# Performance work log

Hardware: AMD Instinct MI355X
Metric: run time of the kernel (lower is better)

Reference implementation:

```python
import jax, jax.numpy as jnp
import numpy as np

BN_EPS = 1e-5


def setup_inputs() -> dict:
    key = jax.random.key(0)
    ks = jax.random.split(key, 13)
    B, C, H, W = 32, 256, 96, 48
    return {
        "x": jax.random.normal(ks[0], (B, C, H, W), dtype=jnp.float32),
        "g_w": jax.random.normal(ks[1], (C,), dtype=jnp.float32),
        "g_b": jax.random.normal(ks[2], (1,), dtype=jnp.float32),
        "theta_w": jax.random.normal(ks[3], (C,), dtype=jnp.float32),
        "theta_b": jax.random.normal(ks[4], (1,), dtype=jnp.float32),
        "phi_w": jax.random.normal(ks[5], (C,), dtype=jnp.float32),
        "phi_b": jax.random.normal(ks[6], (1,), dtype=jnp.float32),
        "W_w": jax.random.normal(ks[7], (C,), dtype=jnp.float32),
        "W_b": jax.random.normal(ks[8], (C,), dtype=jnp.float32),
        "bn_gamma": jax.random.normal(ks[9], (C,), dtype=jnp.float32),
        "bn_beta": jax.random.normal(ks[10], (C,), dtype=jnp.float32),
        "bn_mean": jax.random.normal(ks[11], (C,), dtype=jnp.float32),
        "bn_var": jax.random.uniform(ks[12], (C,), dtype=jnp.float32),
    }


def reference(x, g_w, g_b, theta_w, theta_b, phi_w, phi_b, W_w, W_b,
              bn_gamma, bn_beta, bn_mean, bn_var):
    # x: (B, C, H, W); inter_channels == 1 so all 1x1 convs are channel dots.
    B, C, H, Wd = x.shape
    N = H * Wd
    xf = x.reshape(B, C, N)  # (B, C, N)

    g = jnp.einsum("c,bcn->bn", g_w, xf) + g_b          # (B, N)
    theta = jnp.einsum("c,bcn->bn", theta_w, xf) + theta_b
    phi = jnp.einsum("c,bcn->bn", phi_w, xf) + phi_b

    # f_div_C @ g_x == theta * (phi . g) / N  (rank-1 contraction, exact by associativity)
    s = jnp.sum(phi * g, axis=1) / N                     # (B,)
    y = theta * s[:, None]                               # (B, N), inter_channels dim is 1

    # W: 1x1 conv 1->C, then BatchNorm (inference form), then residual add.
    Wy = y[:, None, :] * W_w[None, :, None] + W_b[None, :, None]  # (B, C, N)
    inv_std = bn_gamma / jnp.sqrt(bn_var + BN_EPS)                 # (C,)
    bn = (Wy - bn_mean[None, :, None]) * inv_std[None, :, None] + bn_beta[None, :, None]

    z = bn.reshape(B, C, H, Wd) + x
    return z
```

## Files before the change

kernel.cpp:

```cpp
#include <hip/hip_runtime.h>

constexpr int Bn = 32;
constexpr int Cn = 256;
constexpr int Hn = 96;
constexpr int Wn = 48;
constexpr int Nn = Hn * Wn;
constexpr int N4 = Nn / 4;
constexpr int TILES = 18;
constexpr float BN_EPS = 1e-5f;

typedef float floatx4 __attribute__((ext_vector_type(4)));

__global__ __launch_bounds__(512) void pass1_kernel(
    const float* __restrict__ x,
    const float* __restrict__ g_w, const float* __restrict__ g_b,
    const float* __restrict__ theta_w, const float* __restrict__ theta_b,
    const float* __restrict__ phi_w, const float* __restrict__ phi_b,
    float* __restrict__ theta_out,
    float* __restrict__ part_out)
{
    __shared__ float wg[Cn], wt[Cn], wp[Cn];
    __shared__ float4 red[3][8][64];

    const int tid  = threadIdx.x;
    const int lane = tid & 63;
    const int wave = tid >> 6;

    if (tid < Cn) {
        wg[tid] = g_w[tid];
        wt[tid] = theta_w[tid];
        wp[tid] = phi_w[tid];
    }
    __syncthreads();

    const int bx   = blockIdx.x;
    const int b    = bx / TILES;
    const int tile = bx % TILES;
    const int n4   = tile * 64 + lane;

    const float4* xb = reinterpret_cast<const float4*>(x)
                     + (size_t)b * (size_t)(Cn * N4) + n4;

    float4 ag = {0.f, 0.f, 0.f, 0.f};
    float4 at = {0.f, 0.f, 0.f, 0.f};
    float4 ap = {0.f, 0.f, 0.f, 0.f};

    const int c0 = wave * 32;
    #pragma unroll 8
    for (int cc = 0; cc < 32; ++cc) {
        const int c = c0 + cc;
        const float4 xv = xb[(size_t)c * N4];
        const float cg = wg[c], ct = wt[c], cp = wp[c];
        ag.x = fmaf(cg, xv.x, ag.x);
        ag.y = fmaf(cg, xv.y, ag.y);
        ag.z = fmaf(cg, xv.z, ag.z);
        ag.w = fmaf(cg, xv.w, ag.w);
        at.x = fmaf(ct, xv.x, at.x);
        at.y = fmaf(ct, xv.y, at.y);
        at.z = fmaf(ct, xv.z, at.z);
        at.w = fmaf(ct, xv.w, at.w);
        ap.x = fmaf(cp, xv.x, ap.x);
        ap.y = fmaf(cp, xv.y, ap.y);
        ap.z = fmaf(cp, xv.z, ap.z);
        ap.w = fmaf(cp, xv.w, ap.w);
    }

    red[0][wave][lane] = ag;
    red[1][wave][lane] = at;
    red[2][wave][lane] = ap;
    __syncthreads();

    if (wave == 0) {
        float4 sg = red[0][0][lane];
        float4 st = red[1][0][lane];
        float4 sp = red[2][0][lane];
        #pragma unroll
        for (int w = 1; w < 8; ++w) {
            const float4 rg = red[0][w][lane];
            const float4 rt = red[1][w][lane];
            const float4 rp = red[2][w][lane];
            sg.x += rg.x; sg.y += rg.y; sg.z += rg.z; sg.w += rg.w;
            st.x += rt.x; st.y += rt.y; st.z += rt.z; st.w += rt.w;
            sp.x += rp.x; sp.y += rp.y; sp.z += rp.z; sp.w += rp.w;
        }

        const float gb = g_b[0], tb = theta_b[0], pb = phi_b[0];

        float4 th;
        th.x = st.x + tb; th.y = st.y + tb; th.z = st.z + tb; th.w = st.w + tb;
        reinterpret_cast<float4*>(theta_out)[(size_t)b * N4 + n4] = th;

        float p = (sg.x + gb) * (sp.x + pb)
                + (sg.y + gb) * (sp.y + pb)
                + (sg.z + gb) * (sp.z + pb)
                + (sg.w + gb) * (sp.w + pb);

        #pragma unroll
        for (int off = 32; off > 0; off >>= 1)
            p += __shfl_down(p, off);

        if (lane == 0)
            part_out[b * TILES + tile] = p;
    }
}

__global__ __launch_bounds__(256) void pass2_kernel(
    const float* __restrict__ x,
    const float* __restrict__ theta_buf,
    const float* __restrict__ part_buf,
    const float* __restrict__ W_w, const float* __restrict__ W_b,
    const float* __restrict__ bn_gamma, const float* __restrict__ bn_beta,
    const float* __restrict__ bn_mean, const float* __restrict__ bn_var,
    float* __restrict__ out)
{
    __shared__ float s_sh;
    const int tid = threadIdx.x;
    const int b   = blockIdx.y;

    if (tid < 64) {
        float p = (tid < TILES) ? part_buf[b * TILES + tid] : 0.0f;
        #pragma unroll
        for (int off = 16; off > 0; off >>= 1)
            p += __shfl_down(p, off);
        if (tid == 0) s_sh = p * (1.0f / (float)Nn);
    }
    __syncthreads();
    const float sb = s_sh;

    const int tg  = blockIdx.x * 256 + tid;
    const int c00 = tg / N4;
    const int n4  = tg - c00 * N4;

    const float4* xb  = reinterpret_cast<const float4*>(x)
                      + (size_t)b * (size_t)(Cn * N4);
    floatx4*      ob  = reinterpret_cast<floatx4*>(out)
                      + (size_t)b * (size_t)(Cn * N4);
    const float4  th  = reinterpret_cast<const float4*>(theta_buf)[(size_t)b * N4 + n4];
    const float   tsx = th.x * sb, tsy = th.y * sb,
                  tsz = th.z * sb, tsw = th.w * sb;

    #pragma unroll
    for (int it = 0; it < Cn / 8; ++it) {
        const int c = c00 + it * 8;
        const float inv_std = bn_gamma[c] * rsqrtf(bn_var[c] + BN_EPS);
        const float a = W_w[c] * inv_std;
        const float d = fmaf(W_b[c] - bn_mean[c], inv_std, bn_beta[c]);

        const size_t idx = (size_t)c * N4 + n4;
        const float4 xv = xb[idx];

        floatx4 o;
        o.x = fmaf(tsx, a, d) + xv.x;
        o.y = fmaf(tsy, a, d) + xv.y;
        o.z = fmaf(tsz, a, d) + xv.z;
        o.w = fmaf(tsw, a, d) + xv.w;

        __builtin_nontemporal_store(o, &ob[idx]);
    }
}

extern "C" void kernel_launch(void* const* d_in, const int* in_sizes, int n_in,
                              void* d_out, int out_size, void* d_ws, size_t ws_size,
                              hipStream_t stream) {
    const float* x        = (const float*)d_in[0];
    const float* g_w      = (const float*)d_in[1];
    const float* g_b      = (const float*)d_in[2];
    const float* theta_w  = (const float*)d_in[3];
    const float* theta_b  = (const float*)d_in[4];
    const float* phi_w    = (const float*)d_in[5];
    const float* phi_b    = (const float*)d_in[6];
    const float* W_w      = (const float*)d_in[7];
    const float* W_b      = (const float*)d_in[8];
    const float* bn_gamma = (const float*)d_in[9];
    const float* bn_beta  = (const float*)d_in[10];
    const float* bn_mean  = (const float*)d_in[11];
    const float* bn_var   = (const float*)d_in[12];

    float* out = (float*)d_out;

    float* theta_buf = (float*)d_ws;
    float* part_buf  = (float*)((char*)d_ws + (size_t)Bn * Nn * sizeof(float));

    pass1_kernel<<<Bn * TILES, 512, 0, stream>>>(
        x, g_w, g_b, theta_w, theta_b, phi_w, phi_b, theta_buf, part_buf);

    dim3 g2(36, Bn);
    pass2_kernel<<<g2, 256, 0, stream>>>(
        x, theta_buf, part_buf, W_w, W_b, bn_gamma, bn_beta, bn_mean, bn_var, out);
}
```

Baseline: 77.07 us.

## Fuse both passes into one persistent cooperative kernel with grid sync

New measurement: 170.0 us. +120.6%, slower.

```diff
diff --git a/kernel.cpp b/kernel.cpp
--- a/kernel.cpp
+++ b/kernel.cpp
@@ -1,4 +1,7 @@
 #include <hip/hip_runtime.h>
+#include <hip/hip_cooperative_groups.h>
+
+namespace cg = cooperative_groups;
 
 constexpr int Bn = 32;
 constexpr int Cn = 256;
@@ -6,10 +9,176 @@
 constexpr int Wn = 48;
 constexpr int Nn = Hn * Wn;
 constexpr int N4 = Nn / 4;
-constexpr int TILES = 18;
+constexpr int TILES_F  = 36;
+constexpr int UNITS    = Bn * TILES_F;
+constexpr int TILES_P1 = 18;
 constexpr float BN_EPS = 1e-5f;
 
 typedef float floatx4 __attribute__((ext_vector_type(4)));
+
+__global__ __launch_bounds__(256, 4) void fused_kernel(
+    const float* __restrict__ x,
+    const float* __restrict__ g_w, const float* __restrict__ g_b,
+    const float* __restrict__ theta_w, const float* __restrict__ theta_b,
+    const float* __restrict__ phi_w, const float* __restrict__ phi_b,
+    const float* __restrict__ W_w, const float* __restrict__ W_b,
+    const float* __restrict__ bn_gamma, const float* __restrict__ bn_beta,
+    const float* __restrict__ bn_mean, const float* __restrict__ bn_var,
+    float* __restrict__ theta_ws,
+    float* __restrict__ part_ws,
+    float* __restrict__ out)
+{
+    __shared__ float wg[Cn], wt[Cn], wp[Cn];
+    __shared__ float a_sh[Cn], d_sh[Cn];
+    __shared__ float4 red_g[4][32], red_t[4][32], red_p[4][32];
+    __shared__ float s_sh;
+
+    const int tid  = threadIdx.x;
+    const int lane = tid & 63;
+    const int wave = tid >> 6;
+    const int n4l  = tid & 31;
+    const int cgrp = tid >> 5;
+    const int c0   = cgrp * 32;
+
+    wg[tid] = g_w[tid];
+    wt[tid] = theta_w[tid];
+    wp[tid] = phi_w[tid];
+    {
+        const float inv_std = bn_gamma[tid] * rsqrtf(bn_var[tid] + BN_EPS);
+        a_sh[tid] = W_w[tid] * inv_std;
+        d_sh[tid] = fmaf(W_b[tid] - bn_mean[tid], inv_std, bn_beta[tid]);
+    }
+    __syncthreads();
+
+    const float gb = g_b[0], tb = theta_b[0], pb = phi_b[0];
+
+    for (int u = blockIdx.x; u < UNITS; u += gridDim.x) {
+        const int b    = u / TILES_F;
+        const int tile = u - b * TILES_F;
+        const int n4   = tile * 32 + n4l;
+
+        const float4* xb = reinterpret_cast<const float4*>(x)
+                         + (size_t)b * (size_t)(Cn * N4) + n4;
+
+        float4 ag = {0.f, 0.f, 0.f, 0.f};
+        float4 at = {0.f, 0.f, 0.f, 0.f};
+        float4 ap = {0.f, 0.f, 0.f, 0.f};
+
+        #pragma unroll 8
+        for (int cc = 0; cc < 32; ++cc) {
+            const int c = c0 + cc;
+            const float4 xv = xb[(size_t)c * N4];
+            const float cg = wg[c], ct = wt[c], cp = wp[c];
+            ag.x = fmaf(cg, xv.x, ag.x);
+            ag.y = fmaf(cg, xv.y, ag.y);
+            ag.z = fmaf(cg, xv.z, ag.z);
+            ag.w = fmaf(cg, xv.w, ag.w);
+            at.x = fmaf(ct, xv.x, at.x);
+            at.y = fmaf(ct, xv.y, at.y);
+            at.z = fmaf(ct, xv.z, at.z);
+            at.w = fmaf(ct, xv.w, at.w);
+            ap.x = fmaf(cp, xv.x, ap.x);
+            ap.y = fmaf(cp, xv.y, ap.y);
+            ap.z = fmaf(cp, xv.z, ap.z);
+            ap.w = fmaf(cp, xv.w, ap.w);
+        }
+
+        ag.x += __shfl_xor(ag.x, 32); ag.y += __shfl_xor(ag.y, 32);
+        ag.z += __shfl_xor(ag.z, 32); ag.w += __shfl_xor(ag.w, 32);
+        at.x += __shfl_xor(at.x, 32); at.y += __shfl_xor(at.y, 32);
+        at.z += __shfl_xor(at.z, 32); at.w += __shfl_xor(at.w, 32);
+        ap.x += __shfl_xor(ap.x, 32); ap.y += __shfl_xor(ap.y, 32);
+        ap.z += __shfl_xor(ap.z, 32); ap.w += __shfl_xor(ap.w, 32);
+
+        if (lane < 32) {
+            red_g[wave][n4l] = ag;
+            red_t[wave][n4l] = at;
+            red_p[wave][n4l] = ap;
+        }
+        __syncthreads();
+
+        if (wave == 0 && lane < 32) {
+            float4 sg = red_g[0][n4l];
+            float4 st = red_t[0][n4l];
+            float4 sp = red_p[0][n4l];
+            #pragma unroll
+            for (int w = 1; w < 4; ++w) {
+                const float4 rg = red_g[w][n4l];
+                const float4 rt = red_t[w][n4l];
+                const float4 rp = red_p[w][n4l];
+                sg.x += rg.x; sg.y += rg.y; sg.z += rg.z; sg.w += rg.w;
+                st.x += rt.x; st.y += rt.y; st.z += rt.z; st.w += rt.w;
+                sp.x += rp.x; sp.y += rp.y; sp.z += rp.z; sp.w += rp.w;
+            }
+
+            float4 th;
+            th.x = st.x + tb; th.y = st.y + tb;
+            th.z = st.z + tb; th.w = st.w + tb;
+            reinterpret_cast<float4*>(theta_ws)[(size_t)b * N4 + n4] = th;
+
+            float p = (sg.x + gb) * (sp.x + pb)
+                    + (sg.y + gb) * (sp.y + pb)
+                    + (sg.z + gb) * (sp.z + pb)
+                    + (sg.w + gb) * (sp.w + pb);
+
+            #pragma unroll
+            for (int off = 16; off > 0; off >>= 1)
+                p += __shfl_down(p, off);
+
+            if (n4l == 0)
+                __hip_atomic_store(&part_ws[b * TILES_F + tile], p,
+                                   __ATOMIC_RELEASE, __HIP_MEMORY_SCOPE_AGENT);
+        }
+        __syncthreads();
+    }
+
+    cg::this_grid().sync();
+
+    for (int u = blockIdx.x; u < UNITS; u += gridDim.x) {
+        const int b    = u / TILES_F;
+        const int tile = u - b * TILES_F;
+        const int n4   = tile * 32 + n4l;
+
+        if (tid < 64) {
+            float p = 0.0f;
+            if (tid < TILES_F)
+                p = __hip_atomic_load(&part_ws[b * TILES_F + tid],
+                                      __ATOMIC_ACQUIRE, __HIP_MEMORY_SCOPE_AGENT);
+            #pragma unroll
+            for (int off = 32; off > 0; off >>= 1)
+                p += __shfl_down(p, off);
+            if (tid == 0) s_sh = p * (1.0f / (float)Nn);
+        }
+        __syncthreads();
+        const float sb = s_sh;
+
+        const float4 th = reinterpret_cast<const float4*>(theta_ws)[(size_t)b * N4 + n4];
+        const float tsx = th.x * sb, tsy = th.y * sb,
+                    tsz = th.z * sb, tsw = th.w * sb;
+
+        const float4* xb = reinterpret_cast<const float4*>(x)
+                         + (size_t)b * (size_t)(Cn * N4) + n4;
+        floatx4* ob = reinterpret_cast<floatx4*>(out)
+                    + (size_t)b * (size_t)(Cn * N4) + n4;
+
+        #pragma unroll 8
+        for (int cc = 0; cc < 32; ++cc) {
+            const int c = c0 + cc;
+            const float a = a_sh[c];
+            const float d = d_sh[c];
+            const float4 xv = xb[(size_t)c * N4];
+
+            floatx4 o;
+            o.x = fmaf(tsx, a, d) + xv.x;
+            o.y = fmaf(tsy, a, d) + xv.y;
+            o.z = fmaf(tsz, a, d) + xv.z;
+            o.w = fmaf(tsw, a, d) + xv.w;
+
+            __builtin_nontemporal_store(o, &ob[(size_t)c * N4]);
+        }
+        __syncthreads();
+    }
+}
 
 __global__ __launch_bounds__(512) void pass1_kernel(
     const float* __restrict__ x,
@@ -34,8 +203,8 @@
     __syncthreads();
 
     const int bx   = blockIdx.x;
-    const int b    = bx / TILES;
-    const int tile = bx % TILES;
+    const int b    = bx / TILES_P1;
+    const int tile = bx % TILES_P1;
     const int n4   = tile * 64 + lane;
 
     const float4* xb = reinterpret_cast<const float4*>(x)
@@ -100,7 +269,7 @@
             p += __shfl_down(p, off);
 
         if (lane == 0)
-            part_out[b * TILES + tile] = p;
+            part_out[b * TILES_P1 + tile] = p;
     }
 }
 
@@ -118,7 +287,7 @@
     const int b   = blockIdx.y;
 
     if (tid < 64) {
-        float p = (tid < TILES) ? part_buf[b * TILES + tid] : 0.0f;
+        float p = (tid < TILES_P1) ? part_buf[b * TILES_P1 + tid] : 0.0f;
         #pragma unroll
         for (int off = 16; off > 0; off >>= 1)
             p += __shfl_down(p, off);
@@ -131,13 +300,13 @@
     const int c00 = tg / N4;
     const int n4  = tg - c00 * N4;
 
-    const float4* xb  = reinterpret_cast<const float4*>(x)
-                      + (size_t)b * (size_t)(Cn * N4);
-    floatx4*      ob  = reinterpret_cast<floatx4*>(out)
-                      + (size_t)b * (size_t)(Cn * N4);
-    const float4  th  = reinterpret_cast<const float4*>(theta_buf)[(size_t)b * N4 + n4];
-    const float   tsx = th.x * sb, tsy = th.y * sb,
-                  tsz = th.z * sb, tsw = th.w * sb;
+    const float4* xb = reinterpret_cast<const float4*>(x)
+                     + (size_t)b * (size_t)(Cn * N4);
+    floatx4*      ob = reinterpret_cast<floatx4*>(out)
+                     + (size_t)b * (size_t)(Cn * N4);
+    const float4  th = reinterpret_cast<const float4*>(theta_buf)[(size_t)b * N4 + n4];
+    const float  tsx = th.x * sb, tsy = th.y * sb,
+                 tsz = th.z * sb, tsw = th.w * sb;
 
     #pragma unroll
     for (int it = 0; it < Cn / 8; ++it) {
@@ -178,13 +347,48 @@
 
     float* out = (float*)d_out;
 
-    float* theta_buf = (float*)d_ws;
-    float* part_buf  = (float*)((char*)d_ws + (size_t)Bn * Nn * sizeof(float));
-
-    pass1_kernel<<<Bn * TILES, 512, 0, stream>>>(
-        x, g_w, g_b, theta_w, theta_b, phi_w, phi_b, theta_buf, part_buf);
-
-    dim3 g2(36, Bn);
-    pass2_kernel<<<g2, 256, 0, stream>>>(
-        x, theta_buf, part_buf, W_w, W_b, bn_gamma, bn_beta, bn_mean, bn_var, out);
+    float* part_buf  = (float*)d_ws;
+    float* theta_buf = (float*)((char*)d_ws + 8192);
+
+    int maxB = 0;
+    hipError_t qerr = hipOccupancyMaxActiveBlocksPerMultiprocessor(
+        &maxB, reinterpret_cast<const void*>(fused_kernel), 256, 0);
+
+    hipError_t lerr = hipErrorUnknown;
+    if (qerr == hipSuccess && maxB > 0) {
+        int nb = maxB * 256;
+        if (nb > UNITS) nb = UNITS;
+
+        void* args[] = {
+            (void*)&x,
+            (void*)&g_w, (void*)&g_b,
+            (void*)&theta_w, (void*)&theta_b,
+            (void*)&phi_w, (void*)&phi_b,
+            (void*)&W_w, (void*)&W_b,
+            (void*)&bn_gamma, (void*)&bn_beta,
+            (void*)&bn_mean, (void*)&bn_var,
+            (void*)&theta_buf, (void*)&part_buf,
+            (void*)&out,
+        };
+
+        lerr = hipLaunchCooperativeKernel(
+            reinterpret_cast<const void*>(fused_kernel),
+            dim3(nb), dim3(256), args, 0u, stream);
+
+        if (lerr != hipSuccess && nb > 256) {
+            lerr = hipLaunchCooperativeKernel(
+                reinterpret_cast<const void*>(fused_kernel),
+                dim3(256), dim3(256), args, 0u, stream);
+        }
+    }
+
+    if (lerr != hipSuccess) {
+        pass1_kernel<<<Bn * TILES_P1, 512, 0, stream>>>(
+            x, g_w, g_b, theta_w, theta_b, phi_w, phi_b, theta_buf, part_buf);
+
+        dim3 g2(36, Bn);
+        pass2_kernel<<<g2, 256, 0, stream>>>(
+            x, theta_buf, part_buf, W_w, W_b,
+            bn_gamma, bn_beta, bn_mean, bn_var, out);
+    }
 }
```

## Retile both passes into small 128-thread blocks, reverse pass2 order for L2 reuse

Applied to the files above, without the earlier changes.

Result: faster. 74.68 us (-3.1%).

```diff
diff --git a/kernel.cpp b/kernel.cpp
--- a/kernel.cpp
+++ b/kernel.cpp
@@ -6,12 +6,13 @@
 constexpr int Wn = 48;
 constexpr int Nn = Hn * Wn;
 constexpr int N4 = Nn / 4;
-constexpr int TILES = 18;
+constexpr int TILES = 72;
+constexpr int NBLK  = Bn * TILES;
 constexpr float BN_EPS = 1e-5f;
 
 typedef float floatx4 __attribute__((ext_vector_type(4)));
 
-__global__ __launch_bounds__(512) void pass1_kernel(
+__global__ __launch_bounds__(128, 5) void pass1_kernel(
     const float* __restrict__ x,
     const float* __restrict__ g_w, const float* __restrict__ g_b,
     const float* __restrict__ theta_w, const float* __restrict__ theta_b,
@@ -20,23 +21,26 @@
     float* __restrict__ part_out)
 {
     __shared__ float wg[Cn], wt[Cn], wp[Cn];
-    __shared__ float4 red[3][8][64];
+    __shared__ float4 xw_g[16], xw_t[16], xw_p[16];
 
     const int tid  = threadIdx.x;
     const int lane = tid & 63;
     const int wave = tid >> 6;
-
-    if (tid < Cn) {
-        wg[tid] = g_w[tid];
-        wt[tid] = theta_w[tid];
-        wp[tid] = phi_w[tid];
+    const int pos  = tid & 15;
+    const int grp  = tid >> 4;
+
+    #pragma unroll
+    for (int i = tid; i < Cn; i += 128) {
+        wg[i] = g_w[i];
+        wt[i] = theta_w[i];
+        wp[i] = phi_w[i];
     }
     __syncthreads();
 
     const int bx   = blockIdx.x;
     const int b    = bx / TILES;
-    const int tile = bx % TILES;
-    const int n4   = tile * 64 + lane;
+    const int tile = bx - b * TILES;
+    const int n4   = tile * 16 + pos;
 
     const float4* xb = reinterpret_cast<const float4*>(x)
                      + (size_t)b * (size_t)(Cn * N4) + n4;
@@ -45,44 +49,61 @@
     float4 at = {0.f, 0.f, 0.f, 0.f};
     float4 ap = {0.f, 0.f, 0.f, 0.f};
 
-    const int c0 = wave * 32;
-    #pragma unroll 8
-    for (int cc = 0; cc < 32; ++cc) {
-        const int c = c0 + cc;
-        const float4 xv = xb[(size_t)c * N4];
-        const float cg = wg[c], ct = wt[c], cp = wp[c];
-        ag.x = fmaf(cg, xv.x, ag.x);
-        ag.y = fmaf(cg, xv.y, ag.y);
-        ag.z = fmaf(cg, xv.z, ag.z);
-        ag.w = fmaf(cg, xv.w, ag.w);
-        at.x = fmaf(ct, xv.x, at.x);
-        at.y = fmaf(ct, xv.y, at.y);
-        at.z = fmaf(ct, xv.z, at.z);
-        at.w = fmaf(ct, xv.w, at.w);
-        ap.x = fmaf(cp, xv.x, ap.x);
-        ap.y = fmaf(cp, xv.y, ap.y);
-        ap.z = fmaf(cp, xv.z, ap.z);
-        ap.w = fmaf(cp, xv.w, ap.w);
-    }
-
-    red[0][wave][lane] = ag;
-    red[1][wave][lane] = at;
-    red[2][wave][lane] = ap;
+    const int c0 = grp * 32;
+    #pragma unroll
+    for (int k = 0; k < 4; ++k) {
+        float4 buf[8];
+        #pragma unroll
+        for (int i = 0; i < 8; ++i)
+            buf[i] = xb[(size_t)(c0 + k * 8 + i) * N4];
+        #pragma unroll
+        for (int i = 0; i < 8; ++i) {
+            const int c = c0 + k * 8 + i;
+            const float cg = wg[c], ct = wt[c], cp = wp[c];
+            const float4 xv = buf[i];
+            ag.x = fmaf(cg, xv.x, ag.x);
+            ag.y = fmaf(cg, xv.y, ag.y);
+            ag.z = fmaf(cg, xv.z, ag.z);
+            ag.w = fmaf(cg, xv.w, ag.w);
+            at.x = fmaf(ct, xv.x, at.x);
+            at.y = fmaf(ct, xv.y, at.y);
+            at.z = fmaf(ct, xv.z, at.z);
+            at.w = fmaf(ct, xv.w, at.w);
+            ap.x = fmaf(cp, xv.x, ap.x);
+            ap.y = fmaf(cp, xv.y, ap.y);
+            ap.z = fmaf(cp, xv.z, ap.z);
+            ap.w = fmaf(cp, xv.w, ap.w);
+        }
+    }
+
+    ag.x += __shfl_xor(ag.x, 16); ag.y += __shfl_xor(ag.y, 16);
+    ag.z += __shfl_xor(ag.z, 16); ag.w += __shfl_xor(ag.w, 16);
+    at.x += __shfl_xor(at.x, 16); at.y += __shfl_xor(at.y, 16);
+    at.z += __shfl_xor(at.z, 16); at.w += __shfl_xor(at.w, 16);
+    ap.x += __shfl_xor(ap.x, 16); ap.y += __shfl_xor(ap.y, 16);
+    ap.z += __shfl_xor(ap.z, 16); ap.w += __shfl_xor(ap.w, 16);
+
+    ag.x += __shfl_xor(ag.x, 32); ag.y += __shfl_xor(ag.y, 32);
+    ag.z += __shfl_xor(ag.z, 32); ag.w += __shfl_xor(ag.w, 32);
+    at.x += __shfl_xor(at.x, 32); at.y += __shfl_xor(at.y, 32);
+    at.z += __shfl_xor(at.z, 32); at.w += __shfl_xor(at.w, 32);
+    ap.x += __shfl_xor(ap.x, 32); ap.y += __shfl_xor(ap.y, 32);
+    ap.z += __shfl_xor(ap.z, 32); ap.w += __shfl_xor(ap.w, 32);
+
+    if (wave == 1 && lane < 16) {
+        xw_g[pos] = ag;
+        xw_t[pos] = at;
+        xw_p[pos] = ap;
+    }
     __syncthreads();
 
-    if (wave == 0) {
-        float4 sg = red[0][0][lane];
-        float4 st = red[1][0][lane];
-        float4 sp = red[2][0][lane];
-        #pragma unroll
-        for (int w = 1; w < 8; ++w) {
-            const float4 rg = red[0][w][lane];
-            const float4 rt = red[1][w][lane];
-            const float4 rp = red[2][w][lane];
-            sg.x += rg.x; sg.y += rg.y; sg.z += rg.z; sg.w += rg.w;
-            st.x += rt.x; st.y += rt.y; st.z += rt.z; st.w += rt.w;
-            sp.x += rp.x; sp.y += rp.y; sp.z += rp.z; sp.w += rp.w;
-        }
+    if (wave == 0 && lane < 16) {
+        const float4 rg = xw_g[pos];
+        const float4 rt = xw_t[pos];
+        const float4 rp = xw_p[pos];
+        float4 sg = {ag.x + rg.x, ag.y + rg.y, ag.z + rg.z, ag.w + rg.w};
+        float4 st = {at.x + rt.x, at.y + rt.y, at.z + rt.z, at.w + rt.w};
+        float4 sp = {ap.x + rp.x, ap.y + rp.y, ap.z + rp.z, ap.w + rp.w};
 
         const float gb = g_b[0], tb = theta_b[0], pb = phi_b[0];
 
@@ -95,16 +116,17 @@
                 + (sg.z + gb) * (sp.z + pb)
                 + (sg.w + gb) * (sp.w + pb);
 
-        #pragma unroll
-        for (int off = 32; off > 0; off >>= 1)
-            p += __shfl_down(p, off);
-
-        if (lane == 0)
+        p += __shfl_down(p, 8);
+        p += __shfl_down(p, 4);
+        p += __shfl_down(p, 2);
+        p += __shfl_down(p, 1);
+
+        if (pos == 0)
             part_out[b * TILES + tile] = p;
     }
 }
 
-__global__ __launch_bounds__(256) void pass2_kernel(
+__global__ __launch_bounds__(128, 5) void pass2_kernel(
     const float* __restrict__ x,
     const float* __restrict__ theta_buf,
     const float* __restrict__ part_buf,
@@ -113,49 +135,71 @@
     const float* __restrict__ bn_mean, const float* __restrict__ bn_var,
     float* __restrict__ out)
 {
+    __shared__ float a_sh[Cn], d_sh[Cn];
     __shared__ float s_sh;
-    const int tid = threadIdx.x;
-    const int b   = blockIdx.y;
+
+    const int tid  = threadIdx.x;
+    const int pos  = tid & 15;
+    const int grp  = tid >> 4;
+
+    const int bx   = (NBLK - 1) - blockIdx.x;
+    const int b    = bx / TILES;
+    const int tile = bx - b * TILES;
+    const int n4   = tile * 16 + pos;
+
+    #pragma unroll
+    for (int i = tid; i < Cn; i += 128) {
+        const float inv_std = bn_gamma[i] * rsqrtf(bn_var[i] + BN_EPS);
+        a_sh[i] = W_w[i] * inv_std;
+        d_sh[i] = fmaf(W_b[i] - bn_mean[i], inv_std, bn_beta[i]);
+    }
 
     if (tid < 64) {
-        float p = (tid < TILES) ? part_buf[b * TILES + tid] : 0.0f;
-        #pragma unroll
-        for (int off = 16; off > 0; off >>= 1)
-            p += __shfl_down(p, off);
+        float p = part_buf[b * TILES + tid];
+        if (tid < TILES - 64)
+            p += part_buf[b * TILES + 64 + tid];
+        p += __shfl_down(p, 32);
+        p += __shfl_down(p, 16);
+        p += __shfl_down(p, 8);
+        p += __shfl_down(p, 4);
+        p += __shfl_down(p, 2);
+        p += __shfl_down(p, 1);
         if (tid == 0) s_sh = p * (1.0f / (float)Nn);
     }
     __syncthreads();
     const float sb = s_sh;
 
-    const int tg  = blockIdx.x * 256 + tid;
-    const int c00 = tg / N4;
-    const int n4  = tg - c00 * N4;
-
-    const float4* xb  = reinterpret_cast<const float4*>(x)
-                      + (size_t)b * (size_t)(Cn * N4);
-    floatx4*      ob  = reinterpret_cast<floatx4*>(out)
-                      + (size_t)b * (size_t)(Cn * N4);
-    const float4  th  = reinterpret_cast<const float4*>(theta_buf)[(size_t)b * N4 + n4];
-    const float   tsx = th.x * sb, tsy = th.y * sb,
-                  tsz = th.z * sb, tsw = th.w * sb;
-
-    #pragma unroll
-    for (int it = 0; it < Cn / 8; ++it) {
-        const int c = c00 + it * 8;
-        const float inv_std = bn_gamma[c] * rsqrtf(bn_var[c] + BN_EPS);
-        const float a = W_w[c] * inv_std;
-        const float d = fmaf(W_b[c] - bn_mean[c], inv_std, bn_beta[c]);
-
-        const size_t idx = (size_t)c * N4 + n4;
-        const float4 xv = xb[idx];
-
-        floatx4 o;
-        o.x = fmaf(tsx, a, d) + xv.x;
-        o.y = fmaf(tsy, a, d) + xv.y;
-        o.z = fmaf(tsz, a, d) + xv.z;
-        o.w = fmaf(tsw, a, d) + xv.w;
-
-        __builtin_nontemporal_store(o, &ob[idx]);
+    const float4 th = reinterpret_cast<const float4*>(theta_buf)[(size_t)b * N4 + n4];
+    const float tsx = th.x * sb, tsy = th.y * sb,
+                tsz = th.z * sb, tsw = th.w * sb;
+
+    const float4* xb = reinterpret_cast<const float4*>(x)
+                     + (size_t)b * (size_t)(Cn * N4) + n4;
+    floatx4* ob = reinterpret_cast<floatx4*>(out)
+                + (size_t)b * (size_t)(Cn * N4) + n4;
+
+    const int c0 = grp * 32;
+    #pragma unroll
+    for (int k = 0; k < 4; ++k) {
+        float4 buf[8];
+        #pragma unroll
+        for (int i = 0; i < 8; ++i)
+            buf[i] = xb[(size_t)(c0 + k * 8 + i) * N4];
+        #pragma unroll
+        for (int i = 0; i < 8; ++i) {
+            const int c = c0 + k * 8 + i;
+            const float a = a_sh[c];
+            const float d = d_sh[c];
+            const float4 xv = buf[i];
+
+            floatx4 o;
+            o.x = fmaf(tsx, a, d) + xv.x;
+            o.y = fmaf(tsy, a, d) + xv.y;
+            o.z = fmaf(tsz, a, d) + xv.z;
+            o.w = fmaf(tsw, a, d) + xv.w;
+
+            __builtin_nontemporal_store(o, &ob[(size_t)c * N4]);
+        }
     }
 }
 
@@ -178,13 +222,13 @@
 
     float* out = (float*)d_out;
 
-    float* theta_buf = (float*)d_ws;
-    float* part_buf  = (float*)((char*)d_ws + (size_t)Bn * Nn * sizeof(float));
-
-    pass1_kernel<<<Bn * TILES, 512, 0, stream>>>(
+    float* part_buf  = (float*)d_ws;
+    float* theta_buf = (float*)((char*)d_ws + 16384);
+
+    pass1_kernel<<<NBLK, 128, 0, stream>>>(
         x, g_w, g_b, theta_w, theta_b, phi_w, phi_b, theta_buf, part_buf);
 
-    dim3 g2(36, Bn);
-    pass2_kernel<<<g2, 256, 0, stream>>>(
-        x, theta_buf, part_buf, W_w, W_b, bn_gamma, bn_beta, bn_mean, bn_var, out);
+    pass2_kernel<<<NBLK, 128, 0, stream>>>(
+        x, theta_buf, part_buf, W_w, W_b,
+        bn_gamma, bn_beta, bn_mean, bn_var, out);
 }
```
